# Kernel tuning notes

Hardware: AMD Instinct MI355X
Metric: run time of the kernel (lower is better)

The kernel has to match this reference:

```python
import jax, jax.numpy as jnp
import numpy as np

N = 100000
E = 1600000
EPS = 1e-5


def _layer_norm(x, g, b):
    mu = jnp.mean(x, axis=-1, keepdims=True)
    var = jnp.mean((x - mu) ** 2, axis=-1, keepdims=True)
    return (x - mu) * jax.lax.rsqrt(var + EPS) * g + b


def _sage(x, src, dst, wl, bl, wr):
    # mean aggregation of neighbor messages x[src] into dst, then linear
    msg_sum = jax.ops.segment_sum(x[src], dst, num_segments=N)          # [N, d_in]
    cnt = jax.ops.segment_sum(jnp.ones((src.shape[0],), x.dtype), dst, num_segments=N)
    mean = msg_sum / jnp.maximum(cnt, 1.0)[:, None]
    return mean @ wl.T + bl + x @ wr.T  # lin_l(mean) + lin_r(x), bias only on lin_l


def setup_inputs() -> dict:
    key = jax.random.key(0)
    ks = jax.random.split(key, 16)
    dims = [(9, 64), (64, 128), (128, 128), (128, 128)]
    inp = {
        "x": jax.random.normal(ks[0], (N, 9), dtype=jnp.float32),
        "edge_index": jax.random.randint(ks[1], (2, E), 0, N, dtype=jnp.int32),
    }
    for i, (din, dout) in enumerate(dims, start=1):
        s = 1.0 / np.sqrt(din)
        inp[f"w{i}l"] = jax.random.uniform(ks[2 + 3 * i], (dout, din), jnp.float32, -s, s)
        inp[f"b{i}"] = jnp.zeros((dout,), jnp.float32)
        inp[f"w{i}r"] = jax.random.uniform(ks[3 + 3 * i], (dout, din), jnp.float32, -s, s)
        inp[f"g{i}"] = jnp.ones((dout,), jnp.float32)
        inp[f"be{i}"] = jnp.zeros((dout,), jnp.float32)
    return inp


def reference(x, edge_index,
              w1l, b1, w1r, g1, be1,
              w2l, b2, w2r, g2, be2,
              w3l, b3, w3r, g3, be3,
              w4l, b4, w4r, g4, be4):
    src, dst = edge_index[0], edge_index[1]
    h = jax.nn.relu(_layer_norm(_sage(x, src, dst, w1l, b1, w1r), g1, be1))
    h = jax.nn.relu(_layer_norm(_sage(h, src, dst, w2l, b2, w2r), g2, be2))
    h = jax.nn.relu(_layer_norm(_sage(h, src, dst, w3l, b3, w3r), g3, be3))
    h = _layer_norm(_sage(h, src, dst, w4l, b4, w4r), g4, be4)
    return h
```

## Files before the change

### kernel.cpp

```cpp
#include <hip/hip_runtime.h>
#include <hip/hip_bf16.h>
#include <math.h>

#define N_NODES 100000
#define EPS 1e-5f
#define B2SH 11
#define NPB2 2048
#define NBUCK2 ((N_NODES + NPB2 - 1) / NPB2)
#define NPART 256

typedef __attribute__((ext_vector_type(8))) short bf16x8;
typedef __attribute__((ext_vector_type(4))) float f32x4;

__device__ __forceinline__ float bflo(unsigned int u) { return __uint_as_float(u << 16); }
__device__ __forceinline__ float bfhi(unsigned int u) { return __uint_as_float(u & 0xffff0000u); }
__device__ __forceinline__ unsigned short fbits(float f) {
    __hip_bfloat16 h = __float2bfloat16(f);
    return *reinterpret_cast<unsigned short*>(&h);
}
__device__ __forceinline__ void stv(float* p, float y) { *p = y; }
__device__ __forceinline__ void stv(__hip_bfloat16* p, float y) { *p = __float2bfloat16(y); }

__global__ void part_hist(const int* __restrict__ dst, int E, int* __restrict__ blkhist) {
    __shared__ int h[NBUCK2];
    int b = blockIdx.x;
    int slice = (E + NPART - 1) / NPART;
    int s0 = b * slice;
    int s1 = min(E, s0 + slice);
    for (int i = threadIdx.x; i < NBUCK2; i += 256) h[i] = 0;
    __syncthreads();
    for (int e = s0 + threadIdx.x; e < s1; e += 256) atomicAdd(&h[dst[e] >> B2SH], 1);
    __syncthreads();
    for (int i = threadIdx.x; i < NBUCK2; i += 256) blkhist[i * NPART + b] = h[i];
}

__global__ void part_offsets(const int* __restrict__ blkhist, int* __restrict__ blkoffs,
                             int* __restrict__ bbase2, int* __restrict__ row_ptr, int E) {
    __shared__ int tot[NBUCK2];
    __shared__ int sbase[NBUCK2 + 1];
    int j = threadIdx.x;
    if (j < NBUCK2) {
        int run = 0;
#pragma unroll 8
        for (int b = 0; b < NPART; ++b) {
            blkoffs[j * NPART + b] = run;
            run += blkhist[j * NPART + b];
        }
        tot[j] = run;
    }
    __syncthreads();
    if (j == 0) {
        int run = 0;
        for (int i = 0; i < NBUCK2; ++i) {
            sbase[i] = run;
            run += tot[i];
        }
        sbase[NBUCK2] = run;
        row_ptr[N_NODES] = E;
    }
    __syncthreads();
    if (j <= NBUCK2) bbase2[j] = sbase[j];
    if (j < NBUCK2) {
        int base = sbase[j];
#pragma unroll 8
        for (int b = 0; b < NPART; ++b) blkoffs[j * NPART + b] += base;
    }
}

__global__ void part_scatter(const int* __restrict__ src, const int* __restrict__ dst, int E,
                             const int* __restrict__ blkoffs, unsigned int* __restrict__ pairs) {
    __shared__ int pos[NBUCK2];
    int b = blockIdx.x;
    int slice = (E + NPART - 1) / NPART;
    int s0 = b * slice;
    int s1 = min(E, s0 + slice);
    for (int i = threadIdx.x; i < NBUCK2; i += 256) pos[i] = blkoffs[i * NPART + b];
    __syncthreads();
    for (int e = s0 + threadIdx.x; e < s1; e += 256) {
        int d = dst[e];
        int jb = d >> B2SH;
        int p = atomicAdd(&pos[jb], 1);
        pairs[p] = ((unsigned int)src[e] << B2SH) | (unsigned int)(d & (NPB2 - 1));
    }
}

__global__ __launch_bounds__(1024) void bucket_build2(const unsigned int* __restrict__ pairs,
                                                      const int* __restrict__ bbase2,
                                                      int* __restrict__ row_ptr,
                                                      int* __restrict__ col) {
    __shared__ int lcnt[NPB2];
    __shared__ int lofs[NPB2];
    __shared__ int part[1024];
    int bk = blockIdx.x;
    int base = bbase2[bk];
    int cntb = bbase2[bk + 1] - base;
    int node0 = bk << B2SH;
    int t = threadIdx.x;
    lcnt[t] = 0;
    lcnt[t + 1024] = 0;
    __syncthreads();
    for (int i = t; i < cntb; i += 1024) atomicAdd(&lcnt[pairs[base + i] & (NPB2 - 1)], 1);
    __syncthreads();
    int a0 = lcnt[2 * t], a1 = lcnt[2 * t + 1];
    part[t] = a0 + a1;
    __syncthreads();
    for (int off = 1; off < 1024; off <<= 1) {
        int v = (t >= off) ? part[t - off] : 0;
        __syncthreads();
        part[t] += v;
        __syncthreads();
    }
    int excl = part[t] - (a0 + a1);
    lofs[2 * t] = excl;
    lofs[2 * t + 1] = excl + a0;
    __syncthreads();
#pragma unroll
    for (int k = 0; k < 2; ++k) {
        int ln = 2 * t + k;
        int node = node0 + ln;
        if (node < N_NODES) row_ptr[node] = base + lofs[ln];
    }
    lcnt[t] = 0;
    lcnt[t + 1024] = 0;
    __syncthreads();
    for (int i = t; i < cntb; i += 1024) {
        unsigned int v = pairs[base + i];
        int ld = v & (NPB2 - 1);
        int s = v >> B2SH;
        int p = base + lofs[ld] + atomicAdd(&lcnt[ld], 1);
        col[p] = s;
    }
}

__global__ void agg9_kernel(const float* __restrict__ x, const int* __restrict__ row_ptr,
                            const int* __restrict__ col, float* __restrict__ mean, int n) {
    int node = (blockIdx.x * blockDim.x + threadIdx.x) >> 6;
    int lane = threadIdx.x & 63;
    int wv = threadIdx.x >> 6;
    __shared__ float red[4][64];
    float acc = 0.f;
    int start = 0, end = 0;
    if (node < n) {
        start = row_ptr[node];
        end = row_ptr[node + 1];
        int g = lane / 9;
        int f = lane - g * 9;
        if (g < 7 && end > start) {
            for (int p = start + g; p < end; p += 28) {
#pragma unroll
                for (int i = 0; i < 4; ++i) {
                    int q = p + i * 7;
                    int idx = (q < end) ? q : end - 1;
                    float v = x[(size_t)col[idx] * 9 + f];
                    if (q >= end) v = 0.f;
                    acc += v;
                }
            }
        }
    }
    red[wv][lane] = acc;
    __syncthreads();
    if (node < n && lane < 9) {
        float s = red[wv][lane];
#pragma unroll
        for (int k = 1; k < 7; ++k) s += red[wv][lane + 9 * k];
        float inv = 1.f / fmaxf((float)(end - start), 1.f);
        mean[(size_t)node * 9 + lane] = s * inv;
    }
}

__global__ void agg64_kernel(const unsigned short* __restrict__ h, const int* __restrict__ row_ptr,
                             const int* __restrict__ col, unsigned short* __restrict__ mean, int n) {
    int node = (blockIdx.x * blockDim.x + threadIdx.x) >> 6;
    int lane = threadIdx.x & 63;
    if (node >= n) return;
    int start = row_ptr[node], end = row_ptr[node + 1];
    int deg = end - start;
    if (deg <= 0) {
        mean[(size_t)node * 64 + lane] = 0;
        return;
    }
    float inv = 1.f / (float)deg;
    float acc = 0.f;
    for (int p = start; p < end; p += 16) {
#pragma unroll
        for (int i = 0; i < 16; ++i) {
            int q = p + i;
            int idx = (q < end) ? q : end - 1;
            unsigned int u = (unsigned int)h[(size_t)col[idx] * 64 + lane];
            if (q >= end) u = 0u;
            acc += bflo(u);
        }
    }
    mean[(size_t)node * 64 + lane] = fbits(acc * inv);
}

__global__ void agg128_kernel(const unsigned short* __restrict__ h, const int* __restrict__ row_ptr,
                              const int* __restrict__ col, unsigned short* __restrict__ mean, int n) {
    int node = (blockIdx.x * blockDim.x + threadIdx.x) >> 6;
    int lane = threadIdx.x & 63;
    if (node >= n) return;
    int start = row_ptr[node], end = row_ptr[node + 1];
    int deg = end - start;
    if (deg <= 0) {
        *(unsigned int*)&mean[(size_t)node * 128 + lane * 2] = 0u;
        return;
    }
    float inv = 1.f / (float)deg;
    float ax = 0.f, ay = 0.f;
    for (int p = start; p < end; p += 16) {
#pragma unroll
        for (int i = 0; i < 16; ++i) {
            int q = p + i;
            int idx = (q < end) ? q : end - 1;
            unsigned int u = *(const unsigned int*)&h[(size_t)col[idx] * 128 + lane * 2];
            if (q >= end) u = 0u;
            ax += bflo(u);
            ay += bfhi(u);
        }
    }
    unsigned int lo = fbits(ax * inv);
    unsigned int hi = fbits(ay * inv);
    *(unsigned int*)&mean[(size_t)node * 128 + lane * 2] = lo | (hi << 16);
}

__global__ void wtrans_kernel(const float* __restrict__ wl, const float* __restrict__ wr,
                              int din, int dout, float* __restrict__ wt) {
    int i = blockIdx.x * blockDim.x + threadIdx.x;
    int K2 = 2 * din;
    if (i >= K2 * dout) return;
    int k = i / dout, j = i % dout;
    wt[k * dout + j] = (k < din) ? wl[j * din + k] : wr[j * din + (k - din)];
}

__global__ void packw_kernel(const float* __restrict__ wl, const float* __restrict__ wr,
                             int din, unsigned short* __restrict__ bpack) {
    int K2 = 2 * din;
    int total = K2 * 128;
    int i = blockIdx.x * 256 + threadIdx.x;
    if (i >= total) return;
    int e = i & 7;
    int lane = (i >> 3) & 63;
    int rest = i >> 9;
    int KSTEPS = din / 16;
    int t = rest / KSTEPS, ks = rest % KSTEPS;
    int j = t * 16 + (lane & 15);
    int k = ks * 32 + (lane >> 4) * 8 + e;
    float w = (k < din) ? wl[j * din + k] : wr[j * din + (k - din)];
    bpack[i] = fbits(w);
}

template <int DIN, int DOUT, bool RELU, typename OT>
__global__ __launch_bounds__(256) void linear_ln_kernel(
    const float* __restrict__ meanp, const float* __restrict__ hp,
    const float* __restrict__ wt, const float* __restrict__ bias,
    const float* __restrict__ g, const float* __restrict__ be,
    OT* __restrict__ out, int n) {
    constexpr int K2 = 2 * DIN;
    constexpr int NCOL = DOUT / 4;
    constexpr int NROW = 256 / NCOL;
    constexpr int TN = 4 * NROW;
    constexpr int ASTR = TN + 4;
    constexpr int OSTR = DOUT + 4;
    constexpr int SMEMF = (K2 * ASTR > TN * OSTR) ? K2 * ASTR : TN * OSTR;
    __shared__ float smem[SMEMF];

    int tid = threadIdx.x;
    int n0base = blockIdx.x * TN;

    for (int idx = tid; idx < TN * K2; idx += 256) {
        int nn = idx / K2;
        int k = idx % K2;
        int node = n0base + nn;
        float v = 0.f;
        if (node < n)
            v = (k < DIN) ? meanp[(size_t)node * DIN + k] : hp[(size_t)node * DIN + (k - DIN)];
        smem[k * ASTR + nn] = v;
    }
    __syncthreads();

    int colt = tid % NCOL;
    int rowt = tid / NCOL;
    int j0 = colt * 4;
    int nn0 = rowt * 4;

    float acc[4][4];
#pragma unroll
    for (int i = 0; i < 4; ++i)
#pragma unroll
        for (int j = 0; j < 4; ++j) acc[i][j] = 0.f;

#pragma unroll 2
    for (int k = 0; k < K2; ++k) {
        float4 a = *(const float4*)&smem[k * ASTR + nn0];
        float4 w = *(const float4*)&wt[k * DOUT + j0];
        acc[0][0] = fmaf(a.x, w.x, acc[0][0]);
        acc[0][1] = fmaf(a.x, w.y, acc[0][1]);
        acc[0][2] = fmaf(a.x, w.z, acc[0][2]);
        acc[0][3] = fmaf(a.x, w.w, acc[0][3]);
        acc[1][0] = fmaf(a.y, w.x, acc[1][0]);
        acc[1][1] = fmaf(a.y, w.y, acc[1][1]);
        acc[1][2] = fmaf(a.y, w.z, acc[1][2]);
        acc[1][3] = fmaf(a.y, w.w, acc[1][3]);
        acc[2][0] = fmaf(a.z, w.x, acc[2][0]);
        acc[2][1] = fmaf(a.z, w.y, acc[2][1]);
        acc[2][2] = fmaf(a.z, w.z, acc[2][2]);
        acc[2][3] = fmaf(a.z, w.w, acc[2][3]);
        acc[3][0] = fmaf(a.w, w.x, acc[3][0]);
        acc[3][1] = fmaf(a.w, w.y, acc[3][1]);
        acc[3][2] = fmaf(a.w, w.z, acc[3][2]);
        acc[3][3] = fmaf(a.w, w.w, acc[3][3]);
    }
    __syncthreads();

    float4 bj = *(const float4*)&bias[j0];
#pragma unroll
    for (int i = 0; i < 4; ++i) {
        float4 o;
        o.x = acc[i][0] + bj.x;
        o.y = acc[i][1] + bj.y;
        o.z = acc[i][2] + bj.z;
        o.w = acc[i][3] + bj.w;
        *(float4*)&smem[(nn0 + i) * OSTR + j0] = o;
    }
    __syncthreads();

    int wid = tid >> 6, lane = tid & 63;
    for (int nn = wid; nn < TN; nn += 4) {
        int node = n0base + nn;
        if (node >= n) continue;
        float v0 = smem[nn * OSTR + lane];
        float v1 = (DOUT == 128) ? smem[nn * OSTR + 64 + lane] : 0.f;
        float s = v0 + v1;
        float ss = v0 * v0 + v1 * v1;
#pragma unroll
        for (int off = 32; off > 0; off >>= 1) {
            s += __shfl_xor(s, off);
            ss += __shfl_xor(ss, off);
        }
        float mu = s / DOUT;
        float var = ss / DOUT - mu * mu;
        float inv = rsqrtf(var + EPS);
        float y0 = (v0 - mu) * inv * g[lane] + be[lane];
        if (RELU) y0 = fmaxf(y0, 0.f);
        stv(&out[(size_t)node * DOUT + lane], y0);
        if (DOUT == 128) {
            float y1 = (v1 - mu) * inv * g[64 + lane] + be[64 + lane];
            if (RELU) y1 = fmaxf(y1, 0.f);
            stv(&out[(size_t)node * DOUT + 64 + lane], y1);
        }
    }
}

template <int DIN, bool RELU, typename OT>
__global__ __launch_bounds__(256) void mfma_linear_ln(
    const unsigned short* __restrict__ meanb, const unsigned short* __restrict__ hb,
    const unsigned short* __restrict__ bpack, const float* __restrict__ bias,
    const float* __restrict__ g, const float* __restrict__ be, OT* __restrict__ out, int n) {
    constexpr int KSTEPS = DIN / 16;
    int tid = threadIdx.x;
    int w = tid >> 6, l = tid & 63;
    int n0 = blockIdx.x * 64 + w * 16;
    int arow = l & 15;
    int koff = (l >> 4) * 8;
    int anode = n0 + arow;
    if (anode >= n) anode = n - 1;
    const unsigned short* mrow = meanb + (size_t)anode * DIN;
    const unsigned short* hrow = hb + (size_t)anode * DIN;

    f32x4 acc[8];
#pragma unroll
    for (int t = 0; t < 8; ++t) acc[t] = (f32x4){0.f, 0.f, 0.f, 0.f};

#pragma unroll
    for (int ks = 0; ks < KSTEPS; ++ks) {
        int k = ks * 32 + koff;
        const unsigned short* ap = (k < DIN) ? (mrow + k) : (hrow + (k - DIN));
        bf16x8 a = *(const bf16x8*)ap;
#pragma unroll
        for (int t = 0; t < 8; ++t) {
            bf16x8 b = *(const bf16x8*)(bpack + (((size_t)t * KSTEPS + ks) * 64 + l) * 8);
            acc[t] = __builtin_amdgcn_mfma_f32_16x16x32_bf16(a, b, acc[t], 0, 0, 0);
        }
    }

    int jbase = l & 15;
    float bj[8], gj[8], bej[8];
#pragma unroll
    for (int t = 0; t < 8; ++t) {
        bj[t] = bias[t * 16 + jbase];
        gj[t] = g[t * 16 + jbase];
        bej[t] = be[t * 16 + jbase];
    }
#pragma unroll
    for (int r = 0; r < 4; ++r) {
        float v[8];
        float s = 0.f, ss = 0.f;
#pragma unroll
        for (int t = 0; t < 8; ++t) {
            v[t] = acc[t][r] + bj[t];
            s += v[t];
            ss += v[t] * v[t];
        }
#pragma unroll
        for (int off = 1; off < 16; off <<= 1) {
            s += __shfl_xor(s, off);
            ss += __shfl_xor(ss, off);
        }
        float mu = s * (1.f / 128.f);
        float var = ss * (1.f / 128.f) - mu * mu;
        float inv = rsqrtf(var + EPS);
        int node = n0 + (l >> 4) * 4 + r;
        if (node < n) {
#pragma unroll
            for (int t = 0; t < 8; ++t) {
                float y = (v[t] - mu) * inv * gj[t] + bej[t];
                if (RELU) y = fmaxf(y, 0.f);
                stv(&out[(size_t)node * 128 + t * 16 + jbase], y);
            }
        }
    }
}

extern "C" void kernel_launch(void* const* d_in, const int* in_sizes, int n_in,
                              void* d_out, int out_size, void* d_ws, size_t ws_size,
                              hipStream_t stream) {
    const float* x = (const float*)d_in[0];
    const int* edge = (const int*)d_in[1];
    int E = in_sizes[1] / 2;
    const int* src = edge;
    const int* dst = edge + E;

    const float* w1l = (const float*)d_in[2];
    const float* b1  = (const float*)d_in[3];
    const float* w1r = (const float*)d_in[4];
    const float* g1  = (const float*)d_in[5];
    const float* be1 = (const float*)d_in[6];
    const float* w2l = (const float*)d_in[7];
    const float* b2  = (const float*)d_in[8];
    const float* w2r = (const float*)d_in[9];
    const float* g2  = (const float*)d_in[10];
    const float* be2 = (const float*)d_in[11];
    const float* w3l = (const float*)d_in[12];
    const float* b3  = (const float*)d_in[13];
    const float* w3r = (const float*)d_in[14];
    const float* g3  = (const float*)d_in[15];
    const float* be3 = (const float*)d_in[16];
    const float* w4l = (const float*)d_in[17];
    const float* b4  = (const float*)d_in[18];
    const float* w4r = (const float*)d_in[19];
    const float* g4  = (const float*)d_in[20];
    const float* be4 = (const float*)d_in[21];

    char* ws = (char*)d_ws;
    size_t off = 0;
    auto alloc = [&](size_t bytes) {
        void* p = ws + off;
        off = (off + bytes + 255) & ~(size_t)255;
        return p;
    };
    int* row_ptr = (int*)alloc((N_NODES + 1) * sizeof(int));
    int* blkhist = (int*)alloc((size_t)NBUCK2 * NPART * sizeof(int));
    int* blkoffs = (int*)alloc((size_t)NBUCK2 * NPART * sizeof(int));
    int* bbase2  = (int*)alloc((NBUCK2 + 1) * sizeof(int));
    unsigned int* pairs = (unsigned int*)alloc((size_t)E * sizeof(unsigned int));
    int* colx    = (int*)alloc((size_t)E * sizeof(int));
    float* wt1   = (float*)alloc(18 * 64 * sizeof(float));
    unsigned short* bp2 = (unsigned short*)alloc(128 * 128 * sizeof(short));
    unsigned short* bp3 = (unsigned short*)alloc(256 * 128 * sizeof(short));
    unsigned short* bp4 = (unsigned short*)alloc(256 * 128 * sizeof(short));
    float* m9    = (float*)alloc((size_t)N_NODES * 9 * sizeof(float));
    unsigned short* mbf = (unsigned short*)alloc((size_t)N_NODES * 128 * sizeof(short));
    unsigned short* h1  = (unsigned short*)alloc((size_t)N_NODES * 64 * sizeof(short));
    unsigned short* h2  = (unsigned short*)alloc((size_t)N_NODES * 128 * sizeof(short));
    unsigned short* h3  = (unsigned short*)alloc((size_t)N_NODES * 128 * sizeof(short));
    (void)ws_size;

    part_hist<<<NPART, 256, 0, stream>>>(dst, E, blkhist);
    part_offsets<<<1, 64, 0, stream>>>(blkhist, blkoffs, bbase2, row_ptr, E);
    part_scatter<<<NPART, 256, 0, stream>>>(src, dst, E, blkoffs, pairs);
    bucket_build2<<<NBUCK2, 1024, 0, stream>>>(pairs, bbase2, row_ptr, colx);

    wtrans_kernel<<<(18 * 64 + 255) / 256, 256, 0, stream>>>(w1l, w1r, 9, 64, wt1);
    packw_kernel<<<(128 * 128 + 255) / 256, 256, 0, stream>>>(w2l, w2r, 64, bp2);
    packw_kernel<<<(256 * 128 + 255) / 256, 256, 0, stream>>>(w3l, w3r, 128, bp3);
    packw_kernel<<<(256 * 128 + 255) / 256, 256, 0, stream>>>(w4l, w4r, 128, bp4);

    float* out = (float*)d_out;
    int AGB = (N_NODES * 64 + 255) / 256;
    int LNB = (N_NODES + 63) / 64;

    agg9_kernel<<<AGB, 256, 0, stream>>>(x, row_ptr, colx, m9, N_NODES);
    linear_ln_kernel<9, 64, true, __hip_bfloat16><<<LNB, 256, 0, stream>>>(
        m9, x, wt1, b1, g1, be1, (__hip_bfloat16*)h1, N_NODES);
    agg64_kernel<<<AGB, 256, 0, stream>>>(h1, row_ptr, colx, mbf, N_NODES);
    mfma_linear_ln<64, true, __hip_bfloat16><<<LNB, 256, 0, stream>>>(
        mbf, h1, bp2, b2, g2, be2, (__hip_bfloat16*)h2, N_NODES);
    agg128_kernel<<<AGB, 256, 0, stream>>>(h2, row_ptr, colx, mbf, N_NODES);
    mfma_linear_ln<128, true, __hip_bfloat16><<<LNB, 256, 0, stream>>>(
        mbf, h2, bp3, b3, g3, be3, (__hip_bfloat16*)h3, N_NODES);
    agg128_kernel<<<AGB, 256, 0, stream>>>(h3, row_ptr, colx, mbf, N_NODES);
    mfma_linear_ln<128, false, float><<<LNB, 256, 0, stream>>>(
        mbf, h3, bp4, b4, g4, be4, out, N_NODES);
}
```

Baseline: 388.4 us.

## Gather neighbor features from an FP8 copy of hidden activations

Each linear+LayerNorm kernel now writes an extra FP8 (e4m3) copy of its output next to the bf16 one. The mean-aggregation kernels gather from this FP8 copy, halving the bytes per neighbor row in the irregular gathers that dominate memory traffic. The aggregation loops are also restructured to unroll by 8 with a separate masked tail instead of a masked 16-way loop. The cost is a less precise aggregated mean, which could breach the accuracy tolerance, plus the extra FP8 writes.

```diff
diff --git a/kernel.cpp b/kernel.cpp
--- a/kernel.cpp
+++ b/kernel.cpp
@@ -20,6 +20,9 @@
 }
 __device__ __forceinline__ void stv(float* p, float y) { *p = y; }
 __device__ __forceinline__ void stv(__hip_bfloat16* p, float y) { *p = __float2bfloat16(y); }
+__device__ __forceinline__ unsigned char f8enc(float y) {
+    return (unsigned char)((unsigned int)__builtin_amdgcn_cvt_pk_fp8_f32(y, y, 0, false) & 0xffu);
+}
 
 __global__ void part_hist(const int* __restrict__ dst, int E, int* __restrict__ blkhist) {
     __shared__ int h[NBUCK2];
@@ -169,7 +172,7 @@
     }
 }
 
-__global__ void agg64_kernel(const unsigned short* __restrict__ h, const int* __restrict__ row_ptr,
+__global__ void agg64_kernel(const unsigned char* __restrict__ h8, const int* __restrict__ row_ptr,
                              const int* __restrict__ col, unsigned short* __restrict__ mean, int n) {
     int node = (blockIdx.x * blockDim.x + threadIdx.x) >> 6;
     int lane = threadIdx.x & 63;
@@ -180,22 +183,33 @@
         mean[(size_t)node * 64 + lane] = 0;
         return;
     }
-    float inv = 1.f / (float)deg;
+    const unsigned char* hl = h8 + lane;
     float acc = 0.f;
-    for (int p = start; p < end; p += 16) {
-#pragma unroll
-        for (int i = 0; i < 16; ++i) {
+    int p = start;
+    int nfull = start + (deg & ~7);
+    for (; p < nfull; p += 8) {
+#pragma unroll
+        for (int i = 0; i < 8; ++i) {
+            unsigned int off = (unsigned int)col[p + i] << 6;
+            unsigned int u = (unsigned int)hl[off];
+            acc += __builtin_amdgcn_cvt_f32_fp8(u, 0);
+        }
+    }
+    if (p < end) {
+#pragma unroll
+        for (int i = 0; i < 8; ++i) {
             int q = p + i;
-            int idx = (q < end) ? q : end - 1;
-            unsigned int u = (unsigned int)h[(size_t)col[idx] * 64 + lane];
-            if (q >= end) u = 0u;
-            acc += bflo(u);
-        }
-    }
-    mean[(size_t)node * 64 + lane] = fbits(acc * inv);
-}
-
-__global__ void agg128_kernel(const unsigned short* __restrict__ h, const int* __restrict__ row_ptr,
+            int idx = (q < end) ? q : p;
+            unsigned int off = (unsigned int)col[idx] << 6;
+            unsigned int u = (unsigned int)hl[off];
+            float v = __builtin_amdgcn_cvt_f32_fp8(u, 0);
+            if (q < end) acc += v;
+        }
+    }
+    mean[(size_t)node * 64 + lane] = fbits(acc / (float)deg);
+}
+
+__global__ void agg128_kernel(const unsigned char* __restrict__ h8, const int* __restrict__ row_ptr,
                               const int* __restrict__ col, unsigned short* __restrict__ mean, int n) {
     int node = (blockIdx.x * blockDim.x + threadIdx.x) >> 6;
     int lane = threadIdx.x & 63;
@@ -206,19 +220,35 @@
         *(unsigned int*)&mean[(size_t)node * 128 + lane * 2] = 0u;
         return;
     }
+    const unsigned char* hl = h8 + lane * 2;
+    float ax = 0.f, ay = 0.f;
+    int p = start;
+    int nfull = start + (deg & ~7);
+    for (; p < nfull; p += 8) {
+#pragma unroll
+        for (int i = 0; i < 8; ++i) {
+            unsigned int off = (unsigned int)col[p + i] << 7;
+            unsigned int u = (unsigned int)*(const unsigned short*)(hl + off);
+            ax += __builtin_amdgcn_cvt_f32_fp8(u, 0);
+            ay += __builtin_amdgcn_cvt_f32_fp8(u, 1);
+        }
+    }
+    if (p < end) {
+#pragma unroll
+        for (int i = 0; i < 8; ++i) {
+            int q = p + i;
+            int idx = (q < end) ? q : p;
+            unsigned int off = (unsigned int)col[idx] << 7;
+            unsigned int u = (unsigned int)*(const unsigned short*)(hl + off);
+            float v0 = __builtin_amdgcn_cvt_f32_fp8(u, 0);
+            float v1 = __builtin_amdgcn_cvt_f32_fp8(u, 1);
+            if (q < end) {
+                ax += v0;
+                ay += v1;
+            }
+        }
+    }
     float inv = 1.f / (float)deg;
-    float ax = 0.f, ay = 0.f;
-    for (int p = start; p < end; p += 16) {
-#pragma unroll
-        for (int i = 0; i < 16; ++i) {
-            int q = p + i;
-            int idx = (q < end) ? q : end - 1;
-            unsigned int u = *(const unsigned int*)&h[(size_t)col[idx] * 128 + lane * 2];
-            if (q >= end) u = 0u;
-            ax += bflo(u);
-            ay += bfhi(u);
-        }
-    }
     unsigned int lo = fbits(ax * inv);
     unsigned int hi = fbits(ay * inv);
     *(unsigned int*)&mean[(size_t)node * 128 + lane * 2] = lo | (hi << 16);
@@ -255,7 +285,7 @@
     const float* __restrict__ meanp, const float* __restrict__ hp,
     const float* __restrict__ wt, const float* __restrict__ bias,
     const float* __restrict__ g, const float* __restrict__ be,
-    OT* __restrict__ out, int n) {
+    OT* __restrict__ out, unsigned char* __restrict__ out8, int n) {
     constexpr int K2 = 2 * DIN;
     constexpr int NCOL = DOUT / 4;
     constexpr int NROW = 256 / NCOL;
@@ -344,10 +374,12 @@
         float y0 = (v0 - mu) * inv * g[lane] + be[lane];
         if (RELU) y0 = fmaxf(y0, 0.f);
         stv(&out[(size_t)node * DOUT + lane], y0);
+        if (out8) out8[(size_t)node * DOUT + lane] = f8enc(y0);
         if (DOUT == 128) {
             float y1 = (v1 - mu) * inv * g[64 + lane] + be[64 + lane];
             if (RELU) y1 = fmaxf(y1, 0.f);
             stv(&out[(size_t)node * DOUT + 64 + lane], y1);
+            if (out8) out8[(size_t)node * DOUT + 64 + lane] = f8enc(y1);
         }
     }
 }
@@ -356,7 +388,8 @@
 __global__ __launch_bounds__(256) void mfma_linear_ln(
     const unsigned short* __restrict__ meanb, const unsigned short* __restrict__ hb,
     const unsigned short* __restrict__ bpack, const float* __restrict__ bias,
-    const float* __restrict__ g, const float* __restrict__ be, OT* __restrict__ out, int n) {
+    const float* __restrict__ g, const float* __restrict__ be, OT* __restrict__ out,
+    unsigned char* __restrict__ out8, int n) {
     constexpr int KSTEPS = DIN / 16;
     int tid = threadIdx.x;
     int w = tid >> 6, l = tid & 63;
@@ -417,6 +450,7 @@
                 float y = (v[t] - mu) * inv * gj[t] + bej[t];
                 if (RELU) y = fmaxf(y, 0.f);
                 stv(&out[(size_t)node * 128 + t * 16 + jbase], y);
+                if (out8) out8[(size_t)node * 128 + t * 16 + jbase] = f8enc(y);
             }
         }
     }
@@ -474,6 +508,9 @@
     unsigned short* h1  = (unsigned short*)alloc((size_t)N_NODES * 64 * sizeof(short));
     unsigned short* h2  = (unsigned short*)alloc((size_t)N_NODES * 128 * sizeof(short));
     unsigned short* h3  = (unsigned short*)alloc((size_t)N_NODES * 128 * sizeof(short));
+    unsigned char* h1f8 = (unsigned char*)alloc((size_t)N_NODES * 64);
+    unsigned char* h2f8 = (unsigned char*)alloc((size_t)N_NODES * 128);
+    unsigned char* h3f8 = (unsigned char*)alloc((size_t)N_NODES * 128);
     (void)ws_size;
 
     part_hist<<<NPART, 256, 0, stream>>>(dst, E, blkhist);
@@ -492,14 +529,14 @@
 
     agg9_kernel<<<AGB, 256, 0, stream>>>(x, row_ptr, colx, m9, N_NODES);
     linear_ln_kernel<9, 64, true, __hip_bfloat16><<<LNB, 256, 0, stream>>>(
-        m9, x, wt1, b1, g1, be1, (__hip_bfloat16*)h1, N_NODES);
-    agg64_kernel<<<AGB, 256, 0, stream>>>(h1, row_ptr, colx, mbf, N_NODES);
+        m9, x, wt1, b1, g1, be1, (__hip_bfloat16*)h1, h1f8, N_NODES);
+    agg64_kernel<<<AGB, 256, 0, stream>>>(h1f8, row_ptr, colx, mbf, N_NODES);
     mfma_linear_ln<64, true, __hip_bfloat16><<<LNB, 256, 0, stream>>>(
-        mbf, h1, bp2, b2, g2, be2, (__hip_bfloat16*)h2, N_NODES);
-    agg128_kernel<<<AGB, 256, 0, stream>>>(h2, row_ptr, colx, mbf, N_NODES);
+        mbf, h1, bp2, b2, g2, be2, (__hip_bfloat16*)h2, h2f8, N_NODES);
+    agg128_kernel<<<AGB, 256, 0, stream>>>(h2f8, row_ptr, colx, mbf, N_NODES);
     mfma_linear_ln<128, true, __hip_bfloat16><<<LNB, 256, 0, stream>>>(
-        mbf, h2, bp3, b3, g3, be3, (__hip_bfloat16*)h3, N_NODES);
-    agg128_kernel<<<AGB, 256, 0, stream>>>(h3, row_ptr, colx, mbf, N_NODES);
+        mbf, h2, bp3, b3, g3, be3, (__hip_bfloat16*)h3, h3f8, N_NODES);
+    agg128_kernel<<<AGB, 256, 0, stream>>>(h3f8, row_ptr, colx, mbf, N_NODES);
     mfma_linear_ln<128, false, float><<<LNB, 256, 0, stream>>>(
-        mbf, h3, bp4, b4, g4, be4, out, N_NODES);
-}
+        mbf, h3, bp4, b4, g4, be4, out, (unsigned char*)nullptr, N_NODES);
+}
```

Result: slower. 404.5 us (+4.2%).
